# Optimization experiments

Measured on AMD Instinct MI355X. Metric: run time of the kernel, lower is better.

## Reference

```python
import jax, jax.numpy as jnp
import numpy as np

OBJ_N, D_KEY, D_VAL, BANK_N, N_Q, BS = 4, 128, 512, 7200, 3600, 1


def setup_inputs() -> dict:
    key = jax.random.key(0)
    k1, k2, k3, k4, k5 = jax.random.split(key, 5)
    return {
        "keys": jax.random.normal(k1, (OBJ_N, D_KEY, BANK_N), dtype=jnp.float32),
        "values": jax.random.normal(k2, (OBJ_N, D_VAL, BANK_N), dtype=jnp.float32),
        "masks": jax.random.uniform(k3, (OBJ_N, 1, BANK_N), dtype=jnp.float32),
        "q_in": jax.random.normal(k4, (BS, D_KEY, N_Q), dtype=jnp.float32),
        "q_out": jax.random.normal(k5, (BS, D_VAL, N_Q), dtype=jnp.float32),
    }


def reference(keys, values, masks, q_in, q_out):
    # keys: (O, Dk, B) memory keys per object; q_in: (S, Dk, N) query keys
    d_key = keys.shape[1]
    scale = 1.0 / jnp.sqrt(jnp.asarray(d_key, dtype=keys.dtype))
    # p[o,s,b,n] = softmax_b( keys[o,:,b] . q_in[s,:,n] / sqrt(Dk) )
    logits = jnp.einsum('odb,sdn->osbn', keys, q_in) * scale
    p = jax.nn.softmax(logits, axis=2)
    # mem[o,s,v,n] = sum_b values[o,v,b] * p[o,s,b,n]
    mem = jnp.einsum('ovb,osbn->osvn', values, p)
    # mask_mem[o,s,1,n]: mask-weighted attention readout, gates q_out
    mask_mem = jnp.einsum('omb,osbn->osmn', masks, p)
    q_out_with_mask = q_out[None] * mask_mem          # (O, S, Dv, N)
    out = jnp.concatenate([mem, q_out_with_mask], axis=2)  # (O, S, 2*Dv, N)
    return jnp.transpose(out, (1, 0, 2, 3))           # (S, O, 2*Dv, N)
```

## Files before the change

kernel.cpp:

```cpp
#include <hip/hip_runtime.h>
#include <hip/hip_bf16.h>

typedef unsigned short u16;
typedef unsigned int   u32;
typedef short bf16x8 __attribute__((ext_vector_type(8)));
typedef float f32x4  __attribute__((ext_vector_type(4)));

#define O_N    4
#define D_K    128
#define D_V    512
#define BANK   7200
#define NQ     3600
#define NT     64
#define BT     32
#define NTILES 57
#define ITERS  (BANK/BT)
#define VH_ROWS 256

#define K_OFF    0
#define V_OFF    16384
#define P_OFF    49152
#define LMM_OFF  53248
#define SMEM_BYTES 53760
#define Q_OFF    V_OFF

#define GLL(gsrc, ldst) __builtin_amdgcn_global_load_lds( \
    (const __attribute__((address_space(1))) void*)(gsrc), \
    (__attribute__((address_space(3))) void*)(ldst), 16, 0, 0)

static __device__ __forceinline__ u16 f2bf(float x) {
    u32 u = __builtin_bit_cast(u32, x);
    return (u16)((u + 0x7FFFu + ((u >> 16) & 1u)) >> 16);
}


__global__ void k_transpose_bf16(const float* __restrict__ in, u16* __restrict__ out) {
    __shared__ float tile[32][33];
    const int obj = blockIdx.z;
    const float* src = in + (size_t)obj * D_K * BANK;
    u16* dst = out + (size_t)obj * BANK * D_K;
    const int bx = blockIdx.x * 32;
    const int by = blockIdx.y * 32;
    const int tx = threadIdx.x, ty = threadIdx.y;
#pragma unroll
    for (int i = 0; i < 4; i++)
        tile[ty + 8 * i][tx] = src[(size_t)(by + ty + 8 * i) * BANK + bx + tx];
    __syncthreads();
#pragma unroll
    for (int i = 0; i < 4; i++)
        dst[(size_t)(bx + ty + 8 * i) * D_K + by + tx] = f2bf(tile[tx][ty + 8 * i]);
}

__global__ void k_convert_bf16(const float* __restrict__ in, u16* __restrict__ out, int n4) {
    int idx = blockIdx.x * blockDim.x + threadIdx.x;
    int stride = gridDim.x * blockDim.x;
    for (int i = idx; i < n4; i += stride) {
        float4 v = reinterpret_cast<const float4*>(in)[i];
        ushort4 o;
        o.x = f2bf(v.x); o.y = f2bf(v.y); o.z = f2bf(v.z); o.w = f2bf(v.w);
        reinterpret_cast<ushort4*>(out)[i] = o;
    }
}

__global__ void k_zero(float* out, int n) {
    int i = blockIdx.x * blockDim.x + threadIdx.x;
    if (i < n) out[i] = 0.f;
}

__launch_bounds__(256, 3)
__global__ void k_matcher(const u16* __restrict__ Kt,
                          const u16* __restrict__ Vb,
                          const float* __restrict__ masks,
                          const float* __restrict__ q_in,
                          const float* __restrict__ q_out,
                          float* __restrict__ out,
                          int G, float* __restrict__ lw, float* __restrict__ mw)
{
    __shared__ __align__(16) char smem[SMEM_BYTES];
    const int tid  = threadIdx.x;
    const int wave = tid >> 6;
    const int lane = tid & 63;
    const int q    = lane >> 4;
    const int lr   = lane & 15;

    const int grp  = blockIdx.x & 7;
    const int o    = grp >> 1;
    const int vh   = grp & 1;
    const int rest = blockIdx.x >> 3;
    const int tile = rest / G;
    const int g    = rest - tile * G;
    const int n0   = tile * NT;
    const int it0  = (ITERS * g) / G;
    const int it1  = (ITERS * (g + 1)) / G;
    const int nit  = it1 - it0;

    for (int idx = tid; idx < NT * D_K; idx += 256) {
        int d = idx >> 6;
        int n = idx & 63;
        int gn = n0 + n;
        float v = (gn < NQ) ? q_in[(size_t)d * NQ + gn] : 0.f;
        int bb = d * 2;
        int sb = n * 256 + ((((bb >> 4) ^ (n & 7)) << 4) | (bb & 15));
        *reinterpret_cast<u16*>(smem + Q_OFF + sb) = f2bf(v);
    }
    __syncthreads();

    bf16x8 qf[4];
    {
        const int n = 16 * wave + lr;
#pragma unroll
        for (int ds = 0; ds < 4; ds++) {
            int gq = (4 * ds + q) ^ (n & 7);
            qf[ds] = *reinterpret_cast<const bf16x8*>(smem + Q_OFF + n * 256 + gq * 16);
        }
    }
    __syncthreads();

    const f32x4 zero4 = {0.f, 0.f, 0.f, 0.f};
    f32x4 acc[4][4];
#pragma unroll
    for (int i = 0; i < 4; i++)
#pragma unroll
        for (int j = 0; j < 4; j++) acc[i][j] = zero4;
    float l_part = 0.f, mm_part = 0.f;
    const float scale = 0.08838834764831845f;

    const u16* Ko = Kt + (size_t)o * BANK * D_K;
    const u16* Vo = Vb + (size_t)o * D_V * BANK + (size_t)vh * VH_ROWS * BANK;
    const float* mPtr = masks + (size_t)o * BANK + it0 * BT + 4 * q;

    const int sK0 = tid, sK1 = tid + 256;
    const u16* kSrc0 = Ko + (size_t)(it0 * BT + (sK0 >> 4)) * D_K + (((sK0 & 15) ^ ((sK0 >> 4) & 7)) << 3);
    const u16* kSrc1 = Ko + (size_t)(it0 * BT + (sK1 >> 4)) * D_K + (((sK1 & 15) ^ ((sK1 >> 4) & 7)) << 3);
#define VSRC(k)  (Vo + (size_t)((tid + (k)*256) >> 2) * BANK + it0 * BT \
                  + ((((tid + (k)*256) & 3) ^ ((((tid + (k)*256) >> 2) ^ ((tid + (k)*256) >> 4)) & 3)) << 3))
    const u16* vSrc0 = VSRC(0);
    const u16* vSrc1 = VSRC(1);
    const u16* vSrc2 = VSRC(2);
    const u16* vSrc3 = VSRC(3);
#undef VSRC

#define ISSUE_STAGE(buf) do {                                              \
        char* kb_ = smem + K_OFF + (buf) * 8192 + wave * 1024;             \
        GLL(kSrc0, kb_);                                                   \
        GLL(kSrc1, kb_ + 4096);                                            \
        char* vb_ = smem + V_OFF + (buf) * 16384 + wave * 1024;            \
        GLL(vSrc0, vb_);                                                   \
        GLL(vSrc1, vb_ + 4096);                                            \
        GLL(vSrc2, vb_ + 8192);                                            \
        GLL(vSrc3, vb_ + 12288);                                           \
        kSrc0 += BT * D_K; kSrc1 += BT * D_K;                              \
        vSrc0 += BT; vSrc1 += BT; vSrc2 += BT; vSrc3 += BT;                \
    } while (0)

    ISSUE_STAGE(0);

    for (int ii = 0; ii < nit; ii++) {
        const int cur = ii & 1;
        asm volatile("s_waitcnt vmcnt(0)" ::: "memory");
        __builtin_amdgcn_s_barrier();
        __builtin_amdgcn_sched_barrier(0);
        if (ii + 1 < nit) ISSUE_STAGE(cur ^ 1);

        const char* kb = smem + K_OFF + cur * 8192;
#pragma unroll
        for (int t = 0; t < 2; t++) {
            f32x4 s_acc = zero4;
            const int b_r = 16 * t + lr;
#pragma unroll
            for (int ds = 0; ds < 4; ds++) {
                int gk = (4 * ds + q) ^ (lr & 7);
                bf16x8 kf = *reinterpret_cast<const bf16x8*>(kb + b_r * 256 + gk * 16);
                s_acc = __builtin_amdgcn_mfma_f32_16x16x32_bf16(kf, qf[ds], s_acc, 0, 0, 0);
            }
            float4 mv = *reinterpret_cast<const float4*>(mPtr + 16 * t);
            float p0 = __expf(s_acc[0] * scale);
            float p1 = __expf(s_acc[1] * scale);
            float p2 = __expf(s_acc[2] * scale);
            float p3 = __expf(s_acc[3] * scale);
            l_part  += p0 + p1 + p2 + p3;
            mm_part += p0 * mv.x + p1 * mv.y + p2 * mv.z + p3 * mv.w;
            ushort4 pk;
            pk.x = f2bf(p0); pk.y = f2bf(p1); pk.z = f2bf(p2); pk.w = f2bf(p3);
            const int n = 16 * wave + lr;
            int gp = (2 * t + (q >> 1)) ^ (n & 3);
            *reinterpret_cast<ushort4*>(smem + P_OFF + n * 64 + gp * 16 + (q & 1) * 8) = pk;
        }
        mPtr += BT;

        asm volatile("s_waitcnt lgkmcnt(0)" ::: "memory");
        __builtin_amdgcn_s_barrier();
        __builtin_amdgcn_sched_barrier(0);

        const char* vb = smem + V_OFF + cur * 16384;
        bf16x8 pf[4];
#pragma unroll
        for (int ng = 0; ng < 4; ng++) {
            int n = 16 * ng + lr;
            pf[ng] = *reinterpret_cast<const bf16x8*>(smem + P_OFF + n * 64 + ((q ^ (n & 3)) << 4));
        }
#pragma unroll
        for (int vt = 0; vt < 4; vt++) {
            int v = 64 * wave + 16 * vt + lr;
            int key = (v ^ (v >> 2)) & 3;
            bf16x8 vf = *reinterpret_cast<const bf16x8*>(vb + v * 64 + ((q ^ key) << 4));
#pragma unroll
            for (int ng = 0; ng < 4; ng++)
                acc[vt][ng] = __builtin_amdgcn_mfma_f32_16x16x32_bf16(vf, pf[ng], acc[vt][ng], 0, 0, 0);
        }
    }

    l_part  += __shfl_xor(l_part, 16);  l_part  += __shfl_xor(l_part, 32);
    mm_part += __shfl_xor(mm_part, 16); mm_part += __shfl_xor(mm_part, 32);
    float* l_lds  = reinterpret_cast<float*>(smem + LMM_OFF);
    float* mm_lds = l_lds + 64;
    if (lane < 16) {
        l_lds[16 * wave + lr]  = l_part;
        mm_lds[16 * wave + lr] = mm_part;
    }
    __syncthreads();

    if (G == 1) {
        float* outo = out + (size_t)o * (1024 * NQ);
#pragma unroll
        for (int ng = 0; ng < 4; ng++) {
            const int n  = 16 * ng + lr;
            const int gn = n0 + n;
            if (gn >= NQ) continue;
            const float invl = 1.f / l_lds[n];
            const float gate = mm_lds[n] * invl;
#pragma unroll
            for (int vt = 0; vt < 4; vt++) {
#pragma unroll
                for (int r = 0; r < 4; r++) {
                    const int v = vh * VH_ROWS + 64 * wave + 16 * vt + 4 * q + r;
                    outo[(size_t)v * NQ + gn] = acc[vt][ng][r] * invl;
                    outo[(size_t)(512 + v) * NQ + gn] = q_out[(size_t)v * NQ + gn] * gate;
                }
            }
        }
    } else {
        float* dst = out + ((size_t)o * 1024 + (size_t)g * 512 + (size_t)vh * VH_ROWS) * NQ;
#pragma unroll
        for (int ng = 0; ng < 4; ng++) {
            const int n  = 16 * ng + lr;
            const int gn = n0 + n;
            if (gn >= NQ) continue;
#pragma unroll
            for (int vt = 0; vt < 4; vt++) {
#pragma unroll
                for (int r = 0; r < 4; r++) {
                    const int v = 64 * wave + 16 * vt + 4 * q + r;
                    dst[(size_t)v * NQ + gn] = acc[vt][ng][r];
                }
            }
        }
        if (vh == 0 && tid < 64) {
            const size_t li = ((size_t)(g * 4 + o) * NTILES + tile) * 64 + tid;
            lw[li] = l_lds[tid];
            mw[li] = mm_lds[tid];
        }
    }
}

__global__ void k_combine(const float* __restrict__ q_out, const float* __restrict__ lw,
                          const float* __restrict__ mw, float* __restrict__ out) {
    const int total = O_N * 512 * (NQ / 4);
    float4* outv = reinterpret_cast<float4*>(out);
    const float4* qv = reinterpret_cast<const float4*>(q_out);
    for (int idx = blockIdx.x * blockDim.x + threadIdx.x; idx < total;
         idx += gridDim.x * blockDim.x) {
        const int o  = idx / (512 * 900);
        const int r  = idx - o * 512 * 900;
        const int v  = r / 900;
        const int g4 = r - v * 900;
        const size_t iA = ((size_t)o * 1024 + v) * 900 + g4;
        const size_t iB = ((size_t)o * 1024 + 512 + v) * 900 + g4;
        float4 A = outv[iA];
        float4 B = outv[iB];
        const int tl = g4 >> 4;
        const int wi = (g4 & 15) * 4;
        const size_t l0i = ((size_t)(0 * 4 + o) * NTILES + tl) * 64 + wi;
        const size_t l1i = ((size_t)(1 * 4 + o) * NTILES + tl) * 64 + wi;
        const float4 l0 = *reinterpret_cast<const float4*>(lw + l0i);
        const float4 l1 = *reinterpret_cast<const float4*>(lw + l1i);
        const float4 m0 = *reinterpret_cast<const float4*>(mw + l0i);
        const float4 m1 = *reinterpret_cast<const float4*>(mw + l1i);
        float4 li, mem, gate;
        li.x = 1.f / (l0.x + l1.x); li.y = 1.f / (l0.y + l1.y);
        li.z = 1.f / (l0.z + l1.z); li.w = 1.f / (l0.w + l1.w);
        mem.x = (A.x + B.x) * li.x; mem.y = (A.y + B.y) * li.y;
        mem.z = (A.z + B.z) * li.z; mem.w = (A.w + B.w) * li.w;
        gate.x = (m0.x + m1.x) * li.x; gate.y = (m0.y + m1.y) * li.y;
        gate.z = (m0.z + m1.z) * li.z; gate.w = (m0.w + m1.w) * li.w;
        float4 qo = qv[(size_t)v * 900 + g4];
        outv[iA] = mem;
        float4 gq;
        gq.x = qo.x * gate.x; gq.y = qo.y * gate.y;
        gq.z = qo.z * gate.z; gq.w = qo.w * gate.w;
        outv[iB] = gq;
    }
}

extern "C" void kernel_launch(void* const* d_in, const int* in_sizes, int n_in,
                              void* d_out, int out_size, void* d_ws, size_t ws_size,
                              hipStream_t stream) {
    const float* keys   = (const float*)d_in[0];
    const float* values = (const float*)d_in[1];
    const float* masks  = (const float*)d_in[2];
    const float* q_in   = (const float*)d_in[3];
    const float* q_outp = (const float*)d_in[4];
    float* out = (float*)d_out;

    const size_t K_BYTES  = (size_t)O_N * BANK * D_K * 2;
    const size_t V_BYTES  = (size_t)O_N * D_V * BANK * 2;
    const size_t LM_FLOATS = (size_t)2 * O_N * NTILES * 64;
    const size_t LM_BYTES  = LM_FLOATS * 4 * 2;

    if (ws_size < K_BYTES + V_BYTES) {
        k_zero<<<(out_size + 255) / 256, 256, 0, stream>>>(out, out_size);
        return;
    }
    const int G = (ws_size >= K_BYTES + V_BYTES + LM_BYTES) ? 2 : 1;

    u16* Kt = (u16*)d_ws;
    u16* Vb = (u16*)((char*)d_ws + K_BYTES);
    float* lw = (float*)((char*)d_ws + K_BYTES + V_BYTES);
    float* mw = lw + LM_FLOATS;

    dim3 tb(32, 8);
    dim3 tg(BANK / 32, D_K / 32, O_N);
    k_transpose_bf16<<<tg, tb, 0, stream>>>(keys, Kt);

    const int n4 = O_N * D_V * BANK / 4;
    k_convert_bf16<<<2048, 256, 0, stream>>>(values, Vb, n4);

    k_matcher<<<NTILES * 8 * G, 256, 0, stream>>>(Kt, Vb, masks, q_in, q_outp, out,
                                                  G, lw, mw);
    if (G == 2)
        k_combine<<<2048, 256, 0, stream>>>(q_outp, lw, mw, out);
}
```

Baseline: 325.7 us.

## Load V fragments directly from global into registers, shrink LDS for occupancy

V tiles no longer pass through double-buffered LDS. Each wave loads its own bf16x8 V fragments straight from global memory into registers at the start of each iteration, and the mask values are prefetched the same way. This cuts LDS use from about 53KB to about 21KB, and launch bounds are raised to 4 blocks per SM so more waves can hide latency. The cost is that V loads are no longer prefetched a stage ahead through LDS, so their global latency sits inside the loop. Register pressure also rises under the tighter occupancy target.

```diff
diff --git a/kernel.cpp b/kernel.cpp
--- a/kernel.cpp
+++ b/kernel.cpp
@@ -18,11 +18,10 @@
 #define VH_ROWS 256
 
 #define K_OFF    0
-#define V_OFF    16384
-#define P_OFF    49152
-#define LMM_OFF  53248
-#define SMEM_BYTES 53760
-#define Q_OFF    V_OFF
+#define P_OFF    16384
+#define LMM_OFF  20480
+#define SMEM_BYTES 20992
+#define Q_OFF    0
 
 #define GLL(gsrc, ldst) __builtin_amdgcn_global_load_lds( \
     (const __attribute__((address_space(1))) void*)(gsrc), \
@@ -67,7 +66,7 @@
     if (i < n) out[i] = 0.f;
 }
 
-__launch_bounds__(256, 3)
+__launch_bounds__(256, 4)
 __global__ void k_matcher(const u16* __restrict__ Kt,
                           const u16* __restrict__ Vb,
                           const float* __restrict__ masks,
@@ -129,38 +128,38 @@
     const u16* Vo = Vb + (size_t)o * D_V * BANK + (size_t)vh * VH_ROWS * BANK;
     const float* mPtr = masks + (size_t)o * BANK + it0 * BT + 4 * q;
 
-    const int sK0 = tid, sK1 = tid + 256;
-    const u16* kSrc0 = Ko + (size_t)(it0 * BT + (sK0 >> 4)) * D_K + (((sK0 & 15) ^ ((sK0 >> 4) & 7)) << 3);
-    const u16* kSrc1 = Ko + (size_t)(it0 * BT + (sK1 >> 4)) * D_K + (((sK1 & 15) ^ ((sK1 >> 4) & 7)) << 3);
-#define VSRC(k)  (Vo + (size_t)((tid + (k)*256) >> 2) * BANK + it0 * BT \
-                  + ((((tid + (k)*256) & 3) ^ ((((tid + (k)*256) >> 2) ^ ((tid + (k)*256) >> 4)) & 3)) << 3))
-    const u16* vSrc0 = VSRC(0);
-    const u16* vSrc1 = VSRC(1);
-    const u16* vSrc2 = VSRC(2);
-    const u16* vSrc3 = VSRC(3);
-#undef VSRC
-
-#define ISSUE_STAGE(buf) do {                                              \
+    const u16* kSrcA = Ko + (size_t)(it0 * BT + (tid >> 4)) * D_K
+                         + (((tid & 15) ^ ((tid >> 4) & 7)) << 3);
+    const u16* kSrcB = Ko + (size_t)(it0 * BT + ((tid + 256) >> 4)) * D_K
+                         + ((((tid + 256) & 15) ^ (((tid + 256) >> 4) & 7)) << 3);
+
+#define ISSUE_K(buf) do {                                                  \
         char* kb_ = smem + K_OFF + (buf) * 8192 + wave * 1024;             \
-        GLL(kSrc0, kb_);                                                   \
-        GLL(kSrc1, kb_ + 4096);                                            \
-        char* vb_ = smem + V_OFF + (buf) * 16384 + wave * 1024;            \
-        GLL(vSrc0, vb_);                                                   \
-        GLL(vSrc1, vb_ + 4096);                                            \
-        GLL(vSrc2, vb_ + 8192);                                            \
-        GLL(vSrc3, vb_ + 12288);                                           \
-        kSrc0 += BT * D_K; kSrc1 += BT * D_K;                              \
-        vSrc0 += BT; vSrc1 += BT; vSrc2 += BT; vSrc3 += BT;                \
+        GLL(kSrcA, kb_);                                                   \
+        GLL(kSrcB, kb_ + 4096);                                            \
+        kSrcA += BT * D_K; kSrcB += BT * D_K;                              \
     } while (0)
 
-    ISSUE_STAGE(0);
+    const u16* Vrow = Vo + it0 * BT;
+    const u32  vOff = (u32)(64 * wave + lr) * BANK + q * 8;
+
+    ISSUE_K(0);
 
     for (int ii = 0; ii < nit; ii++) {
         const int cur = ii & 1;
         asm volatile("s_waitcnt vmcnt(0)" ::: "memory");
         __builtin_amdgcn_s_barrier();
         __builtin_amdgcn_sched_barrier(0);
-        if (ii + 1 < nit) ISSUE_STAGE(cur ^ 1);
+
+        float4 mv0 = *reinterpret_cast<const float4*>(mPtr);
+        float4 mv1 = *reinterpret_cast<const float4*>(mPtr + 16);
+        bf16x8 vf0 = *reinterpret_cast<const bf16x8*>(Vrow + vOff);
+        bf16x8 vf1 = *reinterpret_cast<const bf16x8*>(Vrow + vOff + 16 * BANK);
+        bf16x8 vf2 = *reinterpret_cast<const bf16x8*>(Vrow + vOff + 32 * BANK);
+        bf16x8 vf3 = *reinterpret_cast<const bf16x8*>(Vrow + vOff + 48 * BANK);
+        if (ii + 1 < nit) ISSUE_K(cur ^ 1);
+        mPtr += BT;
+        Vrow += BT;
 
         const char* kb = smem + K_OFF + cur * 8192;
 #pragma unroll
@@ -173,7 +172,7 @@
                 bf16x8 kf = *reinterpret_cast<const bf16x8*>(kb + b_r * 256 + gk * 16);
                 s_acc = __builtin_amdgcn_mfma_f32_16x16x32_bf16(kf, qf[ds], s_acc, 0, 0, 0);
             }
-            float4 mv = *reinterpret_cast<const float4*>(mPtr + 16 * t);
+            const float4 mv = t ? mv1 : mv0;
             float p0 = __expf(s_acc[0] * scale);
             float p1 = __expf(s_acc[1] * scale);
             float p2 = __expf(s_acc[2] * scale);
@@ -186,27 +185,20 @@
             int gp = (2 * t + (q >> 1)) ^ (n & 3);
             *reinterpret_cast<ushort4*>(smem + P_OFF + n * 64 + gp * 16 + (q & 1) * 8) = pk;
         }
-        mPtr += BT;
 
         asm volatile("s_waitcnt lgkmcnt(0)" ::: "memory");
         __builtin_amdgcn_s_barrier();
         __builtin_amdgcn_sched_barrier(0);
 
-        const char* vb = smem + V_OFF + cur * 16384;
-        bf16x8 pf[4];
 #pragma unroll
         for (int ng = 0; ng < 4; ng++) {
             int n = 16 * ng + lr;
-            pf[ng] = *reinterpret_cast<const bf16x8*>(smem + P_OFF + n * 64 + ((q ^ (n & 3)) << 4));
-        }
-#pragma unroll
-        for (int vt = 0; vt < 4; vt++) {
-            int v = 64 * wave + 16 * vt + lr;
-            int key = (v ^ (v >> 2)) & 3;
-            bf16x8 vf = *reinterpret_cast<const bf16x8*>(vb + v * 64 + ((q ^ key) << 4));
-#pragma unroll
-            for (int ng = 0; ng < 4; ng++)
-                acc[vt][ng] = __builtin_amdgcn_mfma_f32_16x16x32_bf16(vf, pf[ng], acc[vt][ng], 0, 0, 0);
+            bf16x8 pf = *reinterpret_cast<const bf16x8*>(
+                smem + P_OFF + n * 64 + ((q ^ (n & 3)) << 4));
+            acc[0][ng] = __builtin_amdgcn_mfma_f32_16x16x32_bf16(vf0, pf, acc[0][ng], 0, 0, 0);
+            acc[1][ng] = __builtin_amdgcn_mfma_f32_16x16x32_bf16(vf1, pf, acc[1][ng], 0, 0, 0);
+            acc[2][ng] = __builtin_amdgcn_mfma_f32_16x16x32_bf16(vf2, pf, acc[2][ng], 0, 0, 0);
+            acc[3][ng] = __builtin_amdgcn_mfma_f32_16x16x32_bf16(vf3, pf, acc[3][ng], 0, 0, 0);
         }
     }
 
```

Measured after the change: 627.0 us. 92.5% more time.
